# Performance work log

Hardware: AMD Instinct MI355X
Metric: run time of the kernel (lower is better)

The kernel has to match this reference:

```python
import jax, jax.numpy as jnp
import numpy as np

N_HEAD = 16
NEG_BIG = 1e10


def setup_inputs() -> dict:
    key = jax.random.key(0)
    ks = jax.random.split(key, 4)
    B, T, D = 2, 2048, 1024
    x = jax.random.normal(ks[0], (B, T, D), dtype=jnp.float32)
    w_attn = jax.random.normal(ks[1], (D, 3 * D), dtype=jnp.float32) * 0.02
    b_attn = jnp.zeros((3 * D,), dtype=jnp.float32)
    w_proj = jax.random.normal(ks[2], (D, D), dtype=jnp.float32) * 0.02
    b_proj = jnp.zeros((D,), dtype=jnp.float32)
    return {"x": x, "w_attn": w_attn, "b_attn": b_attn, "w_proj": w_proj, "b_proj": b_proj}


def reference(x, w_attn, b_attn, w_proj, b_proj):
    B, T, D = x.shape
    H = N_HEAD
    dh = D // H
    # fused QKV projection (Conv1d == addmm: x @ W + b)
    qkv = x @ w_attn + b_attn                      # [B, T, 3D]
    q, k, v = jnp.split(qkv, 3, axis=-1)
    # split heads -> [B, H, T, dh]
    q = q.reshape(B, T, H, dh).transpose(0, 2, 1, 3)
    k = k.reshape(B, T, H, dh).transpose(0, 2, 1, 3)
    v = v.reshape(B, T, H, dh).transpose(0, 2, 1, 3)
    # scores; repo scales by 1/sqrt(n_head) (its idiosyncrasy, kept faithfully)
    w = jnp.einsum('bhqd,bhkd->bhqk', q, k) / jnp.sqrt(jnp.float32(H))
    # causal mask via repo formula: w*b - 1e10*(1-b), b = tril ones
    b = jnp.tril(jnp.ones((T, T), dtype=w.dtype))
    w = w * b - NEG_BIG * (1.0 - b)
    w = jax.nn.softmax(w, axis=-1)
    a = jnp.einsum('bhqk,bhkd->bhqd', w, v)        # [B, H, T, dh]
    # merge heads
    a = a.transpose(0, 2, 1, 3).reshape(B, T, D)
    a = a @ w_proj + b_proj
    present = jnp.stack([k, v])                     # [2, B, H, T, dh]
    return a, present
```

## Files before the change

kernel.cpp:

```cpp
#include <hip/hip_runtime.h>
#include <hip/hip_bf16.h>

typedef __hip_bfloat16 bf16;
typedef unsigned short ush;
typedef __attribute__((ext_vector_type(8))) short bf16x8;
typedef __attribute__((ext_vector_type(4))) float f32x4;

#define BB 2
#define TT 2048
#define DD 1024
#define HH 16
#define DHH 64
#define MM (BB*TT)
#define N3 (3*DD)

__device__ __forceinline__ bf16  f2b(float x){ return __float2bfloat16(x); }
__device__ __forceinline__ ush   f2bu(float x){ bf16 h = __float2bfloat16(x); return *(ush*)&h; }

__global__ __launch_bounds__(256) void transpose_cvt(
    const float* __restrict__ src, ush* __restrict__ dst, int R, int C)
{
    __shared__ ush T[64][68];
    const int tid = threadIdx.x;
    const int c0 = blockIdx.x * 64;
    const int r0 = blockIdx.y * 64;

    #pragma unroll
    for (int it = 0; it < 4; it++) {
        int idx = it * 256 + tid;
        int i = idx >> 4, jf = idx & 15;
        float4 v = *(const float4*)&src[(size_t)(r0 + i) * C + c0 + jf * 4];
        T[jf * 4 + 0][i] = f2bu(v.x);
        T[jf * 4 + 1][i] = f2bu(v.y);
        T[jf * 4 + 2][i] = f2bu(v.z);
        T[jf * 4 + 3][i] = f2bu(v.w);
    }
    __syncthreads();
    #pragma unroll
    for (int it = 0; it < 4; it++) {
        int idx = it * 256 + tid;
        int j = idx >> 4, i4 = idx & 15;
        *(ushort4*)&dst[(size_t)(c0 + j) * R + r0 + i4 * 4] =
            *(const ushort4*)&T[j][i4 * 4];
    }
}

__global__ __launch_bounds__(256) void qkv_mfma(
    const float* __restrict__ x, const ush* __restrict__ wT,
    const float* __restrict__ bias,
    bf16* __restrict__ qws, float* __restrict__ kout, float* __restrict__ vout,
    ush* __restrict__ kbf, ush* __restrict__ vtb, int write_bf)
{
    __shared__ __align__(16) ush As[128][40];
    __shared__ __align__(16) ush Bs[128][40];

    const int tid  = threadIdx.x;
    const int lane = tid & 63;
    const int w    = tid >> 6;
    const int n16  = lane & 15;
    const int quad = lane >> 4;
    const int row0 = blockIdx.y * 128;
    const int col0 = blockIdx.x * 128;
    const int wrow = (w >> 1) * 64;
    const int wcol = (w & 1) * 64;

    f32x4 acc[4][4];
    #pragma unroll
    for (int mb = 0; mb < 4; mb++)
        #pragma unroll
        for (int nb = 0; nb < 4; nb++) acc[mb][nb] = (f32x4){0.f,0.f,0.f,0.f};

    for (int kk0 = 0; kk0 < DD; kk0 += 32) {
        __syncthreads();
        #pragma unroll
        for (int it = 0; it < 4; it++) {
            int idx = it * 256 + tid;
            int m = idx >> 3, kf = idx & 7;
            float4 v = *(const float4*)&x[(size_t)(row0 + m) * DD + kk0 + kf * 4];
            ushort4 u;
            u.x = f2bu(v.x); u.y = f2bu(v.y); u.z = f2bu(v.z); u.w = f2bu(v.w);
            *(ushort4*)&As[m][kf * 4] = u;
        }
        #pragma unroll
        for (int it = 0; it < 2; it++) {
            int idx = it * 256 + tid;
            int n = idx >> 2, kc = idx & 3;
            *(bf16x8*)&Bs[n][kc * 8] =
                *(const bf16x8*)&wT[(size_t)(col0 + n) * DD + kk0 + kc * 8];
        }
        __syncthreads();

        bf16x8 af[4];
        #pragma unroll
        for (int mb = 0; mb < 4; mb++)
            af[mb] = *(const bf16x8*)&As[wrow + mb * 16 + n16][quad * 8];
        #pragma unroll
        for (int nb = 0; nb < 4; nb++) {
            bf16x8 bfr = *(const bf16x8*)&Bs[wcol + nb * 16 + n16][quad * 8];
            #pragma unroll
            for (int mb = 0; mb < 4; mb++)
                acc[mb][nb] = __builtin_amdgcn_mfma_f32_16x16x32_bf16(
                    af[mb], bfr, acc[mb][nb], 0, 0, 0);
        }
    }

    #pragma unroll
    for (int nb = 0; nb < 4; nb++) {
        const int gc = col0 + wcol + nb * 16 + n16;
        const float bv = bias[gc];
        const int which = gc >> 10;
        const int h = (gc & 1023) >> 6;
        const int d = gc & 63;
        #pragma unroll
        for (int mb = 0; mb < 4; mb++) {
            float vv[4];
            #pragma unroll
            for (int reg = 0; reg < 4; reg++) vv[reg] = acc[mb][nb][reg] + bv;
            const int gr0 = row0 + wrow + mb * 16 + quad * 4;
            const int b_ = gr0 >> 11, t0 = gr0 & 2047;
            const int bh = b_ * HH + h;
            const size_t tbase = ((size_t)bh * TT + t0) * DHH + d;
            if (which == 0) {
                #pragma unroll
                for (int reg = 0; reg < 4; reg++)
                    qws[tbase + (size_t)reg * DHH] = f2b(vv[reg]);
            } else if (which == 1) {
                #pragma unroll
                for (int reg = 0; reg < 4; reg++) kout[tbase + (size_t)reg * DHH] = vv[reg];
                if (write_bf) {
                    #pragma unroll
                    for (int reg = 0; reg < 4; reg++)
                        kbf[tbase + (size_t)reg * DHH] = f2bu(vv[reg]);
                }
            } else {
                #pragma unroll
                for (int reg = 0; reg < 4; reg++) vout[tbase + (size_t)reg * DHH] = vv[reg];
                if (write_bf) {
                    ushort4 u;
                    u.x = f2bu(vv[0]); u.y = f2bu(vv[1]);
                    u.z = f2bu(vv[2]); u.w = f2bu(vv[3]);
                    *(ushort4*)&vtb[((size_t)bh * DHH + d) * TT + t0] = u;
                }
            }
        }
    }
}

__global__ __launch_bounds__(256) void flash_attn_v3(
    const ush* __restrict__ qin, const ush* __restrict__ kbf,
    const ush* __restrict__ vtb, bf16* __restrict__ attn)
{
    __shared__ __align__(16) ush Ks[64][72];
    __shared__ __align__(16) ush Vt[64][72];
    __shared__ __align__(16) ush Ps[4][16][72];

    const int tid  = threadIdx.x;
    const int lane = tid & 63;
    const int w    = tid >> 6;
    const int n16  = lane & 15;
    const int quad = lane >> 4;
    const int bh = blockIdx.y;
    const int qi = (bh & 8) ? (31 - (int)blockIdx.x) : (int)blockIdx.x;
    const int q0 = qi * 64;
    const ush* Qb  = qin + (size_t)bh * TT * DHH;
    const ush* Kb  = kbf + (size_t)bh * TT * DHH;
    const ush* Vtb = vtb + (size_t)bh * DHH * TT;
    const int b_ = bh >> 4, h = bh & 15;

    const ush* Qp = Qb + (size_t)(q0 + w * 16 + n16) * DHH + quad * 8;
    const bf16x8 qa0 = *(const bf16x8*)&Qp[0];
    const bf16x8 qa1 = *(const bf16x8*)&Qp[32];

    const int r0c = tid >> 3, c8c = (tid & 7) * 8;
    const int r1c = (256 + tid) >> 3, c8c1 = ((256 + tid) & 7) * 8;

    bf16x8 kst[2], vst[2];
    {
        const ush* Kp = Kb;
        const ush* Vp = Vtb;
        kst[0] = *(const bf16x8*)&Kp[(size_t)r0c * DHH + c8c];
        kst[1] = *(const bf16x8*)&Kp[(size_t)r1c * DHH + c8c1];
        vst[0] = *(const bf16x8*)&Vp[(size_t)r0c * TT + c8c];
        vst[1] = *(const bf16x8*)&Vp[(size_t)r1c * TT + c8c1];
    }

    f32x4 o[4];
    #pragma unroll
    for (int db = 0; db < 4; db++) o[db] = (f32x4){0.f, 0.f, 0.f, 0.f};
    float lsum[4] = {0.f, 0.f, 0.f, 0.f};

    const int grow_base = q0 + w * 16 + quad * 4;
    const float SC = 0.25f * 1.4426950408889634f;

    for (int kt = 0; kt <= qi; kt++) {
        __syncthreads();
        *(bf16x8*)&Ks[r0c][c8c]  = kst[0];
        *(bf16x8*)&Ks[r1c][c8c1] = kst[1];
        *(bf16x8*)&Vt[r0c][c8c]  = vst[0];
        *(bf16x8*)&Vt[r1c][c8c1] = vst[1];
        __syncthreads();

        if (kt < qi) {
            const ush* Kp = Kb + (size_t)((kt + 1) * 64) * DHH;
            const ush* Vp = Vtb + (kt + 1) * 64;
            kst[0] = *(const bf16x8*)&Kp[(size_t)r0c * DHH + c8c];
            kst[1] = *(const bf16x8*)&Kp[(size_t)r1c * DHH + c8c1];
            vst[0] = *(const bf16x8*)&Vp[(size_t)r0c * TT + c8c];
            vst[1] = *(const bf16x8*)&Vp[(size_t)r1c * TT + c8c1];
        }

        f32x4 s[4];
        #pragma unroll
        for (int cb = 0; cb < 4; cb++) {
            bf16x8 kb0 = *(const bf16x8*)&Ks[cb * 16 + n16][quad * 8];
            bf16x8 kb1 = *(const bf16x8*)&Ks[cb * 16 + n16][32 + quad * 8];
            f32x4 acc = (f32x4){0.f, 0.f, 0.f, 0.f};
            acc = __builtin_amdgcn_mfma_f32_16x16x32_bf16(qa0, kb0, acc, 0, 0, 0);
            acc = __builtin_amdgcn_mfma_f32_16x16x32_bf16(qa1, kb1, acc, 0, 0, 0);
            s[cb] = acc;
        }

        const int gcol_base = kt * 64 + n16;
        #pragma unroll
        for (int reg = 0; reg < 4; reg++) {
            #pragma unroll
            for (int cb = 0; cb < 4; cb++) {
                float p = exp2f(s[cb][reg] * SC);
                if (gcol_base + cb * 16 > grow_base + reg) p = 0.f;
                lsum[reg] += p;
                Ps[w][quad * 4 + reg][cb * 16 + n16] = f2bu(p);
            }
        }

        bf16x8 pa0 = *(const bf16x8*)&Ps[w][n16][quad * 8];
        bf16x8 pa1 = *(const bf16x8*)&Ps[w][n16][32 + quad * 8];
        #pragma unroll
        for (int db = 0; db < 4; db++) {
            bf16x8 vb0 = *(const bf16x8*)&Vt[db * 16 + n16][quad * 8];
            bf16x8 vb1 = *(const bf16x8*)&Vt[db * 16 + n16][32 + quad * 8];
            o[db] = __builtin_amdgcn_mfma_f32_16x16x32_bf16(pa0, vb0, o[db], 0, 0, 0);
            o[db] = __builtin_amdgcn_mfma_f32_16x16x32_bf16(pa1, vb1, o[db], 0, 0, 0);
        }
    }

    #pragma unroll
    for (int reg = 0; reg < 4; reg++) {
        float ls = lsum[reg];
        #pragma unroll
        for (int off = 1; off < 16; off <<= 1)
            ls += __shfl_xor(ls, off);
        const float il = 1.0f / ls;
        const int t_ = grow_base + reg;
        bf16* outr = attn + ((size_t)(b_ * TT + t_)) * DD + h * 64 + n16;
        #pragma unroll
        for (int db = 0; db < 4; db++)
            outr[db * 16] = f2b(o[db][reg] * il);
    }
}

__global__ __launch_bounds__(256) void flash_attn_mfma(
    const bf16* __restrict__ qin, const float* __restrict__ kin,
    const float* __restrict__ vin, bf16* __restrict__ attn)
{
    __shared__ __align__(16) ush Qs[64][72];
    __shared__ __align__(16) ush Ks[64][72];
    __shared__ __align__(16) ush Vt[64][72];
    __shared__ __align__(16) ush Ps[4][16][72];

    const int tid  = threadIdx.x;
    const int lane = tid & 63;
    const int w    = tid >> 6;
    const int n16  = lane & 15;
    const int quad = lane >> 4;
    const int qi = blockIdx.x;
    const int bh = blockIdx.y;
    const int q0 = qi * 64;

    const ush*   Qp = (const ush*)qin + ((size_t)bh * TT + q0) * DHH;
    const float* Kb = kin + (size_t)bh * TT * DHH;
    const float* Vb = vin + (size_t)bh * TT * DHH;

    #pragma unroll
    for (int it = 0; it < 4; it++) {
        int idx = (it * 256 + tid) * 4;
        int r = idx >> 6, d = idx & 63;
        *(ushort4*)&Qs[r][d] = *(const ushort4*)&Qp[idx];
    }

    f32x4 o[4];
    #pragma unroll
    for (int db = 0; db < 4; db++) o[db] = (f32x4){0.f, 0.f, 0.f, 0.f};
    float m_old[4] = {-1e30f, -1e30f, -1e30f, -1e30f};
    float l_run[4] = {0.f, 0.f, 0.f, 0.f};

    for (int kt = 0; kt <= qi; kt++) {
        const float* Kp = Kb + (size_t)(kt * 64) * DHH;
        const float* Vp = Vb + (size_t)(kt * 64) * DHH;
        __syncthreads();
        #pragma unroll
        for (int it = 0; it < 4; it++) {
            int idx = (it * 256 + tid) * 4;
            int c = idx >> 6, d = idx & 63;
            float4 kv = *(const float4*)&Kp[idx];
            ushort4 kb;
            kb.x = f2bu(kv.x); kb.y = f2bu(kv.y); kb.z = f2bu(kv.z); kb.w = f2bu(kv.w);
            *(ushort4*)&Ks[c][d] = kb;
        }
        #pragma unroll
        for (int it = 0; it < 4; it++) {
            int c = tid & 63, d0 = (tid >> 6) * 4 + it * 16;
            float4 vv = *(const float4*)&Vp[c * 64 + d0];
            Vt[d0 + 0][c] = f2bu(vv.x);
            Vt[d0 + 1][c] = f2bu(vv.y);
            Vt[d0 + 2][c] = f2bu(vv.z);
            Vt[d0 + 3][c] = f2bu(vv.w);
        }
        __syncthreads();

        bf16x8 qa0 = *(const bf16x8*)&Qs[w * 16 + n16][quad * 8];
        bf16x8 qa1 = *(const bf16x8*)&Qs[w * 16 + n16][32 + quad * 8];
        f32x4 s[4];
        #pragma unroll
        for (int cb = 0; cb < 4; cb++) {
            bf16x8 kb0 = *(const bf16x8*)&Ks[cb * 16 + n16][quad * 8];
            bf16x8 kb1 = *(const bf16x8*)&Ks[cb * 16 + n16][32 + quad * 8];
            f32x4 acc = (f32x4){0.f, 0.f, 0.f, 0.f};
            acc = __builtin_amdgcn_mfma_f32_16x16x32_bf16(qa0, kb0, acc, 0, 0, 0);
            acc = __builtin_amdgcn_mfma_f32_16x16x32_bf16(qa1, kb1, acc, 0, 0, 0);
            s[cb] = acc;
        }

        const int grow_base = q0 + w * 16 + quad * 4;
        const int gcol_base = kt * 64 + n16;
        #pragma unroll
        for (int reg = 0; reg < 4; reg++) {
            float sv[4];
            float pm = -1e30f;
            #pragma unroll
            for (int cb = 0; cb < 4; cb++) {
                float v = s[cb][reg] * 0.25f;
                if (gcol_base + cb * 16 > grow_base + reg) v = -1e10f;
                sv[cb] = v;
                pm = fmaxf(pm, v);
            }
            #pragma unroll
            for (int off = 1; off < 16; off <<= 1)
                pm = fmaxf(pm, __shfl_xor(pm, off));
            float mnew = fmaxf(m_old[reg], pm);
            float alpha = __expf(m_old[reg] - mnew);
            float ps = 0.f;
            #pragma unroll
            for (int cb = 0; cb < 4; cb++) {
                float p = __expf(sv[cb] - mnew);
                Ps[w][quad * 4 + reg][cb * 16 + n16] = f2bu(p);
                ps += p;
            }
            #pragma unroll
            for (int off = 1; off < 16; off <<= 1)
                ps += __shfl_xor(ps, off);
            l_run[reg] = l_run[reg] * alpha + ps;
            m_old[reg] = mnew;
            #pragma unroll
            for (int db = 0; db < 4; db++) o[db][reg] *= alpha;
        }
        __syncthreads();

        bf16x8 pa0 = *(const bf16x8*)&Ps[w][n16][quad * 8];
        bf16x8 pa1 = *(const bf16x8*)&Ps[w][n16][32 + quad * 8];
        #pragma unroll
        for (int db = 0; db < 4; db++) {
            bf16x8 vb0 = *(const bf16x8*)&Vt[db * 16 + n16][quad * 8];
            bf16x8 vb1 = *(const bf16x8*)&Vt[db * 16 + n16][32 + quad * 8];
            o[db] = __builtin_amdgcn_mfma_f32_16x16x32_bf16(pa0, vb0, o[db], 0, 0, 0);
            o[db] = __builtin_amdgcn_mfma_f32_16x16x32_bf16(pa1, vb1, o[db], 0, 0, 0);
        }
    }

    const int b_ = bh >> 4, h = bh & 15;
    #pragma unroll
    for (int reg = 0; reg < 4; reg++) {
        const float il = 1.0f / l_run[reg];
        const int t_ = q0 + w * 16 + quad * 4 + reg;
        bf16* outr = attn + ((size_t)(b_ * TT + t_)) * DD + h * 64 + n16;
        #pragma unroll
        for (int db = 0; db < 4; db++)
            outr[db * 16] = f2b(o[db][reg] * il);
    }
}

__global__ __launch_bounds__(256) void proj_mfma(
    const ush* __restrict__ a, const ush* __restrict__ wpT,
    const float* __restrict__ bias, float* __restrict__ out)
{
    __shared__ __align__(16) ush As[128][40];
    __shared__ __align__(16) ush Bs[128][40];

    const int tid  = threadIdx.x;
    const int lane = tid & 63;
    const int w    = tid >> 6;
    const int n16  = lane & 15;
    const int quad = lane >> 4;
    const int row0 = blockIdx.y * 128;
    const int col0 = blockIdx.x * 128;
    const int wrow = (w >> 1) * 64;
    const int wcol = (w & 1) * 64;

    f32x4 acc[4][4];
    #pragma unroll
    for (int mb = 0; mb < 4; mb++)
        #pragma unroll
        for (int nb = 0; nb < 4; nb++) acc[mb][nb] = (f32x4){0.f,0.f,0.f,0.f};

    for (int kk0 = 0; kk0 < DD; kk0 += 32) {
        __syncthreads();
        #pragma unroll
        for (int it = 0; it < 2; it++) {
            int idx = it * 256 + tid;
            int m = idx >> 2, kc = idx & 3;
            *(bf16x8*)&As[m][kc * 8] =
                *(const bf16x8*)&a[(size_t)(row0 + m) * DD + kk0 + kc * 8];
        }
        #pragma unroll
        for (int it = 0; it < 2; it++) {
            int idx = it * 256 + tid;
            int n = idx >> 2, kc = idx & 3;
            *(bf16x8*)&Bs[n][kc * 8] =
                *(const bf16x8*)&wpT[(size_t)(col0 + n) * DD + kk0 + kc * 8];
        }
        __syncthreads();

        bf16x8 af[4];
        #pragma unroll
        for (int mb = 0; mb < 4; mb++)
            af[mb] = *(const bf16x8*)&As[wrow + mb * 16 + n16][quad * 8];
        #pragma unroll
        for (int nb = 0; nb < 4; nb++) {
            bf16x8 bfr = *(const bf16x8*)&Bs[wcol + nb * 16 + n16][quad * 8];
            #pragma unroll
            for (int mb = 0; mb < 4; mb++)
                acc[mb][nb] = __builtin_amdgcn_mfma_f32_16x16x32_bf16(
                    af[mb], bfr, acc[mb][nb], 0, 0, 0);
        }
    }

    #pragma unroll
    for (int nb = 0; nb < 4; nb++) {
        const int gc = col0 + wcol + nb * 16 + n16;
        const float bv = bias[gc];
        #pragma unroll
        for (int mb = 0; mb < 4; mb++) {
            #pragma unroll
            for (int reg = 0; reg < 4; reg++) {
                const int gr = row0 + wrow + mb * 16 + quad * 4 + reg;
                out[(size_t)gr * DD + gc] = acc[mb][nb][reg] + bv;
            }
        }
    }
}

extern "C" void kernel_launch(void* const* d_in, const int* in_sizes, int n_in,
                              void* d_out, int out_size, void* d_ws, size_t ws_size,
                              hipStream_t stream) {
    const float *x = nullptr, *w_attn = nullptr, *b_attn = nullptr,
                *w_proj = nullptr, *b_proj = nullptr;
    for (int i = 0; i < n_in; i++) {
        switch (in_sizes[i]) {
            case 4194304: x      = (const float*)d_in[i]; break;
            case 3145728: w_attn = (const float*)d_in[i]; break;
            case 3072:    b_attn = (const float*)d_in[i]; break;
            case 1048576: w_proj = (const float*)d_in[i]; break;
            case 1024:    b_proj = (const float*)d_in[i]; break;
            default: break;
        }
    }
    if (!x || !w_attn || !b_attn || !w_proj || !b_proj) return;

    float* out_a = (float*)d_out;
    float* out_k = out_a + (size_t)MM * DD;
    float* out_v = out_k + (size_t)BB * HH * TT * DHH;

    const size_t MB = 1024 * 1024;
    char* wsc = (char*)d_ws;
    ush*  wT     = (ush*)(wsc + 0);
    bf16* attnws = (bf16*)(wsc + 0);
    bf16* qws    = (bf16*)(wsc + 8 * MB);
    ush*  wpT    = (ush*)(wsc + 8 * MB);

    if (ws_size >= 32 * MB) {
        ush* kbf = (ush*)(wsc + 16 * MB);
        ush* vtb = (ush*)(wsc + 24 * MB);
        transpose_cvt<<<dim3(N3 / 64, DD / 64), 256, 0, stream>>>(w_attn, wT, DD, N3);
        qkv_mfma<<<dim3(N3 / 128, MM / 128), 256, 0, stream>>>(
            x, wT, b_attn, qws, out_k, out_v, kbf, vtb, 1);
        flash_attn_v3<<<dim3(TT / 64, BB * HH), 256, 0, stream>>>(
            (const ush*)qws, kbf, vtb, attnws);
        transpose_cvt<<<dim3(DD / 64, DD / 64), 256, 0, stream>>>(w_proj, wpT, DD, DD);
        proj_mfma<<<dim3(DD / 128, MM / 128), 256, 0, stream>>>(
            (const ush*)attnws, wpT, b_proj, out_a);
    } else if (ws_size >= 16 * MB) {
        transpose_cvt<<<dim3(N3 / 64, DD / 64), 256, 0, stream>>>(w_attn, wT, DD, N3);
        qkv_mfma<<<dim3(N3 / 128, MM / 128), 256, 0, stream>>>(
            x, wT, b_attn, qws, out_k, out_v, nullptr, nullptr, 0);
        flash_attn_mfma<<<dim3(TT / 64, BB * HH), 256, 0, stream>>>(
            qws, out_k, out_v, attnws);
        transpose_cvt<<<dim3(DD / 64, DD / 64), 256, 0, stream>>>(w_proj, wpT, DD, DD);
        proj_mfma<<<dim3(DD / 128, MM / 128), 256, 0, stream>>>(
            (const ush*)attnws, wpT, b_proj, out_a);
    }
}
```

Baseline: 212.8 us.

## Pre-convert x to bf16 and stage GEMM tiles via direct global-to-LDS loads

Adds a kernel that converts x to bf16 once, using the output buffer as scratch, so the QKV GEMM no longer converts fp32 to bf16 inside every tile load. Both GEMMs now fill shared memory with direct global-to-LDS 16-byte loads into unpadded 32-wide tiles, skipping the register round trip. The unpadded layout may cause LDS bank conflicts on fragment reads, and the extra conversion pass adds an fp32 read and a bf16 write of x.

```diff
diff --git a/kernel.cpp b/kernel.cpp
--- a/kernel.cpp
+++ b/kernel.cpp
@@ -16,6 +16,23 @@
 
 __device__ __forceinline__ bf16  f2b(float x){ return __float2bfloat16(x); }
 __device__ __forceinline__ ush   f2bu(float x){ bf16 h = __float2bfloat16(x); return *(ush*)&h; }
+
+#define GLOAD_LDS(gp, lp) \
+    __builtin_amdgcn_global_load_lds( \
+        (const __attribute__((address_space(1))) void*)(gp), \
+        (__attribute__((address_space(3))) void*)(lp), 16, 0, 0)
+
+__global__ __launch_bounds__(256) void cvt_x(
+    const float* __restrict__ src, ush* __restrict__ dst)
+{
+    const size_t i = ((size_t)blockIdx.x * 256 + threadIdx.x) * 8;
+    float4 a = *(const float4*)&src[i];
+    float4 b = *(const float4*)&src[i + 4];
+    ushort4 u0; u0.x = f2bu(a.x); u0.y = f2bu(a.y); u0.z = f2bu(a.z); u0.w = f2bu(a.w);
+    ushort4 u1; u1.x = f2bu(b.x); u1.y = f2bu(b.y); u1.z = f2bu(b.z); u1.w = f2bu(b.w);
+    *(ushort4*)&dst[i] = u0;
+    *(ushort4*)&dst[i + 4] = u1;
+}
 
 __global__ __launch_bounds__(256) void transpose_cvt(
     const float* __restrict__ src, ush* __restrict__ dst, int R, int C)
@@ -46,13 +63,13 @@
 }
 
 __global__ __launch_bounds__(256) void qkv_mfma(
-    const float* __restrict__ x, const ush* __restrict__ wT,
+    const ush* __restrict__ xbf, const ush* __restrict__ wT,
     const float* __restrict__ bias,
     bf16* __restrict__ qws, float* __restrict__ kout, float* __restrict__ vout,
     ush* __restrict__ kbf, ush* __restrict__ vtb, int write_bf)
 {
-    __shared__ __align__(16) ush As[128][40];
-    __shared__ __align__(16) ush Bs[128][40];
+    __shared__ __align__(16) ush As[128 * 32];
+    __shared__ __align__(16) ush Bs[128 * 32];
 
     const int tid  = threadIdx.x;
     const int lane = tid & 63;
@@ -73,30 +90,21 @@
     for (int kk0 = 0; kk0 < DD; kk0 += 32) {
         __syncthreads();
         #pragma unroll
-        for (int it = 0; it < 4; it++) {
-            int idx = it * 256 + tid;
-            int m = idx >> 3, kf = idx & 7;
-            float4 v = *(const float4*)&x[(size_t)(row0 + m) * DD + kk0 + kf * 4];
-            ushort4 u;
-            u.x = f2bu(v.x); u.y = f2bu(v.y); u.z = f2bu(v.z); u.w = f2bu(v.w);
-            *(ushort4*)&As[m][kf * 4] = u;
-        }
-        #pragma unroll
         for (int it = 0; it < 2; it++) {
-            int idx = it * 256 + tid;
-            int n = idx >> 2, kc = idx & 3;
-            *(bf16x8*)&Bs[n][kc * 8] =
-                *(const bf16x8*)&wT[(size_t)(col0 + n) * DD + kk0 + kc * 8];
+            int c = it * 256 + tid;
+            int r = c >> 2, co = (c & 3) * 8;
+            GLOAD_LDS(&xbf[(size_t)(row0 + r) * DD + kk0 + co], &As[c * 8]);
+            GLOAD_LDS(&wT[(size_t)(col0 + r) * DD + kk0 + co], &Bs[c * 8]);
         }
         __syncthreads();
 
         bf16x8 af[4];
         #pragma unroll
         for (int mb = 0; mb < 4; mb++)
-            af[mb] = *(const bf16x8*)&As[wrow + mb * 16 + n16][quad * 8];
+            af[mb] = *(const bf16x8*)&As[(wrow + mb * 16 + n16) * 32 + quad * 8];
         #pragma unroll
         for (int nb = 0; nb < 4; nb++) {
-            bf16x8 bfr = *(const bf16x8*)&Bs[wcol + nb * 16 + n16][quad * 8];
+            bf16x8 bfr = *(const bf16x8*)&Bs[(wcol + nb * 16 + n16) * 32 + quad * 8];
             #pragma unroll
             for (int mb = 0; mb < 4; mb++)
                 acc[mb][nb] = __builtin_amdgcn_mfma_f32_16x16x32_bf16(
@@ -392,8 +400,8 @@
     const ush* __restrict__ a, const ush* __restrict__ wpT,
     const float* __restrict__ bias, float* __restrict__ out)
 {
-    __shared__ __align__(16) ush As[128][40];
-    __shared__ __align__(16) ush Bs[128][40];
+    __shared__ __align__(16) ush As[128 * 32];
+    __shared__ __align__(16) ush Bs[128 * 32];
 
     const int tid  = threadIdx.x;
     const int lane = tid & 63;
@@ -415,27 +423,20 @@
         __syncthreads();
         #pragma unroll
         for (int it = 0; it < 2; it++) {
-            int idx = it * 256 + tid;
-            int m = idx >> 2, kc = idx & 3;
-            *(bf16x8*)&As[m][kc * 8] =
-                *(const bf16x8*)&a[(size_t)(row0 + m) * DD + kk0 + kc * 8];
-        }
-        #pragma unroll
-        for (int it = 0; it < 2; it++) {
-            int idx = it * 256 + tid;
-            int n = idx >> 2, kc = idx & 3;
-            *(bf16x8*)&Bs[n][kc * 8] =
-                *(const bf16x8*)&wpT[(size_t)(col0 + n) * DD + kk0 + kc * 8];
+            int c = it * 256 + tid;
+            int r = c >> 2, co = (c & 3) * 8;
+            GLOAD_LDS(&a[(size_t)(row0 + r) * DD + kk0 + co], &As[c * 8]);
+            GLOAD_LDS(&wpT[(size_t)(col0 + r) * DD + kk0 + co], &Bs[c * 8]);
         }
         __syncthreads();
 
         bf16x8 af[4];
         #pragma unroll
         for (int mb = 0; mb < 4; mb++)
-            af[mb] = *(const bf16x8*)&As[wrow + mb * 16 + n16][quad * 8];
+            af[mb] = *(const bf16x8*)&As[(wrow + mb * 16 + n16) * 32 + quad * 8];
         #pragma unroll
         for (int nb = 0; nb < 4; nb++) {
-            bf16x8 bfr = *(const bf16x8*)&Bs[wcol + nb * 16 + n16][quad * 8];
+            bf16x8 bfr = *(const bf16x8*)&Bs[(wcol + nb * 16 + n16) * 32 + quad * 8];
             #pragma unroll
             for (int mb = 0; mb < 4; mb++)
                 acc[mb][nb] = __builtin_amdgcn_mfma_f32_16x16x32_bf16(
@@ -485,22 +486,25 @@
     bf16* attnws = (bf16*)(wsc + 0);
     bf16* qws    = (bf16*)(wsc + 8 * MB);
     ush*  wpT    = (ush*)(wsc + 8 * MB);
+    ush*  xbf    = (ush*)d_out;
 
     if (ws_size >= 32 * MB) {
         ush* kbf = (ush*)(wsc + 16 * MB);
         ush* vtb = (ush*)(wsc + 24 * MB);
+        cvt_x<<<dim3(MM * DD / (256 * 8)), 256, 0, stream>>>(x, xbf);
         transpose_cvt<<<dim3(N3 / 64, DD / 64), 256, 0, stream>>>(w_attn, wT, DD, N3);
         qkv_mfma<<<dim3(N3 / 128, MM / 128), 256, 0, stream>>>(
-            x, wT, b_attn, qws, out_k, out_v, kbf, vtb, 1);
+            xbf, wT, b_attn, qws, out_k, out_v, kbf, vtb, 1);
         flash_attn_v3<<<dim3(TT / 64, BB * HH), 256, 0, stream>>>(
             (const ush*)qws, kbf, vtb, attnws);
         transpose_cvt<<<dim3(DD / 64, DD / 64), 256, 0, stream>>>(w_proj, wpT, DD, DD);
         proj_mfma<<<dim3(DD / 128, MM / 128), 256, 0, stream>>>(
             (const ush*)attnws, wpT, b_proj, out_a);
     } else if (ws_size >= 16 * MB) {
+        cvt_x<<<dim3(MM * DD / (256 * 8)), 256, 0, stream>>>(x, xbf);
         transpose_cvt<<<dim3(N3 / 64, DD / 64), 256, 0, stream>>>(w_attn, wT, DD, N3);
         qkv_mfma<<<dim3(N3 / 128, MM / 128), 256, 0, stream>>>(
-            x, wT, b_attn, qws, out_k, out_v, nullptr, nullptr, 0);
+            xbf, wT, b_attn, qws, out_k, out_v, nullptr, nullptr, 0);
         flash_attn_mfma<<<dim3(TT / 64, BB * HH), 256, 0, stream>>>(
             qws, out_k, out_v, attnws);
         transpose_cvt<<<dim3(DD / 64, DD / 64), 256, 0, stream>>>(w_proj, wpT, DD, DD);
```

Result: faster. 204.1 us (-4.1%).
